# Kernel tuning notes

Hardware: AMD Instinct MI355X
Metric: run time of the kernel (lower is better)

## Reference

```python
import jax, jax.numpy as jnp
import numpy as np

N, C, R, P1, P2 = 8, 3, 8, 512, 512
EPS = 1e-10


def setup_inputs() -> dict:
    key = jax.random.key(0)
    k1, k2, k3, k4 = jax.random.split(key, 4)
    X = jax.random.uniform(k1, (N, C, P1, P2), dtype=jnp.float32)
    S = jax.random.uniform(k2, (C, R), dtype=jnp.float32)
    # mimic the learned-init normalization: unit-norm columns of S
    S = S / jnp.linalg.norm(S, axis=0, keepdims=True)
    gamma = jax.random.uniform(k3, (1,), dtype=jnp.float32) * 1e-5
    lam = jax.random.uniform(k4, (1,), dtype=jnp.float32) * 1e-5
    return {"X": X, "S": S, "gamma": gamma, "lam": lam, "n_iter": 3}


def reference(X, S, gamma, lam, n_iter):
    n, c, p1, p2 = X.shape
    r = S.shape[1]
    p = p1 * p2
    X = X.reshape(n, c, p)
    gamma = jnp.abs(gamma)  # (1,)
    lam = jnp.abs(lam)      # (1,)
    Dt = jnp.zeros((n, r, p), dtype=X.dtype)
    x0 = jnp.mean(X, axis=2, keepdims=True)
    for _ in range(n_iter):
        # ---- D update (proximal gradient) ----
        SDt = jnp.einsum('cr,nrp->ncp', S, Dt)                    # [n,c,p]
        x0 = jnp.mean(X + SDt, axis=2, keepdims=True)             # [n,c,1]
        tau_D = 1.0 / jnp.sum(S * S)                              # 1/||S||_F^2
        Dt = Dt - tau_D * (jnp.einsum('cr,ncp->nrp', S, SDt + X)
                           - jnp.einsum('cr,ncq->nrq', S, x0))
        S_nrm = jnp.linalg.norm(S, axis=0).reshape(1, r, 1)       # col L2 norms of S
        Dt = jax.nn.relu(Dt - lam * gamma * tau_D * S_nrm)        # L1 prox
        Dt_L2 = jnp.linalg.norm(Dt, axis=2, keepdims=True)        # [n,r,1]
        scl = jax.nn.relu(Dt_L2 - lam * tau_D * S_nrm)
        scl = scl / Dt_L2 + EPS                                   # faithful to source
        Dt = Dt * scl                                             # L2 (group) prox
        # ---- S update (proximal gradient) ----
        SDt = jnp.einsum('cr,nrp->ncp', S, Dt)
        x0 = jnp.mean(X + SDt, axis=2, keepdims=True)             # [n,c,1]
        Dt_sum = jnp.sum(Dt, axis=2, keepdims=True)               # [n,r,1]
        tau_S = 1.0 / jnp.mean(jnp.sum(Dt * Dt, axis=(1, 2)))     # 1/mean ||Dt_i||_F^2
        G = (jnp.einsum('ncp,nrp->ncr', SDt + X, Dt)
             - x0 @ jnp.swapaxes(Dt_sum, 1, 2))                   # [n,c,r]
        S_grad = S - tau_S * jnp.mean(G, axis=0)                  # [c,r]
        Dt_nrm = jnp.mean(gamma * jnp.sum(jnp.abs(Dt), axis=2, keepdims=True)
                          + jnp.linalg.norm(Dt, axis=2, keepdims=True), axis=0)  # [r,1]
        S_nrm2 = jnp.linalg.norm(S_grad, axis=0, keepdims=True)   # [1,r]
        scl_S = jax.nn.relu(S_nrm2 - lam * tau_S * Dt_nrm.T)
        scl_S = scl_S / (S_nrm2 + EPS)
        S = S_grad * scl_S
        # ---- unit-norm rescaling of S columns ----
        S_nrm3 = jnp.linalg.norm(S, axis=0, keepdims=True)        # [1,r]
        S = S / (S_nrm3 + EPS)
        Dt = Dt * (S_nrm3.reshape(1, r, 1) + EPS)
    return (x0, S, Dt.reshape(n, r, p1, p2))
```

## Files before the change

### kernel.cpp

```cpp
#include <hip/hip_runtime.h>
#include <math.h>

#define N_ 8
#define C_ 3
#define R_ 8
#define P_ 262144
#define P4_ 65536
#define EPS_ 1e-10f
#define INVP_ (1.0f / (float)P_)
#define NRED 68

#define NBLK_X 64
#define NTHR_  (NBLK_X * 256)
#define NBLK_F 256

#define WS_MXP 0
#define WS_RED 1536
#define WS_POST 3200
#define PSLOT(it) (WS_POST + (it) * 176)
#define WS_DTB 4096
#define WS_NEED_BYTES ((size_t)16384 + (size_t)N_ * R_ * P_ * 2)

struct PostLds {
    float sS[C_][R_];
    float sMx[N_][C_];
    float sTh[R_];
    float sB[N_][R_];
    float sAl[N_][R_];
    float sSumD[N_][R_];
    float sGm[N_][R_][R_ + 1];
    float sXd[N_][C_][R_];
    float sScl[N_][R_];
    float sX0[N_][C_];
    float sTau[1];
};

__device__ __forceinline__ float bf2f(unsigned short s) {
    return __uint_as_float(((unsigned)s) << 16);
}
__device__ __forceinline__ unsigned short f2bf(float f, float* back) {
    unsigned u = __float_as_uint(f);
    unsigned r = (u + 0x7FFFu + ((u >> 16) & 1u)) & 0xFFFF0000u;
    *back = __uint_as_float(r);
    return (unsigned short)(r >> 16);
}

__device__ void prologue(PostLds& L, int it,
                         const float* __restrict__ S_in,
                         const float* __restrict__ gammap,
                         const float* __restrict__ lamp,
                         float* __restrict__ out, float* __restrict__ ws)
{
    const int t = threadIdx.x;
    const int r_l = t & 7, n_l = (t >> 3) & 7;
    const float gamma = fabsf(gammap[0]);
    const float lam   = fabsf(lamp[0]);

    if (t < 24) {
        float s = 0.f;
#pragma unroll
        for (int b = 0; b < 64; ++b) s += ws[WS_MXP + t * 64 + b];
        L.sMx[t / C_][t % C_] = s * INVP_;
    }
    if (t < 24)
        L.sS[t / R_][t % R_] = (it <= 1) ? S_in[t] : ws[PSLOT(it - 1) + t];
    __syncthreads();

    if (it == 0) {
        float ss = 0.f;
#pragma unroll
        for (int c = 0; c < C_; ++c)
#pragma unroll
            for (int rr = 0; rr < R_; ++rr) ss += L.sS[c][rr] * L.sS[c][rr];
        const float tauD0 = 1.f / ss;
        if (t == 0) L.sTau[0] = tauD0;
        if (t < R_) {
            float sn = sqrtf(L.sS[0][t]*L.sS[0][t] + L.sS[1][t]*L.sS[1][t] + L.sS[2][t]*L.sS[2][t]);
            L.sTh[t] = lam * gamma * tauD0 * sn;
        }
        if (t < 64) {
            float b = 0.f;
#pragma unroll
            for (int c = 0; c < C_; ++c) b += L.sS[c][r_l] * L.sMx[n_l][c];
            L.sB[n_l][r_l] = b;
            L.sAl[n_l][r_l] = 0.f;
        }
        __syncthreads();
        return;
    }

    float ssp = 0.f;
#pragma unroll
    for (int c = 0; c < C_; ++c)
#pragma unroll
        for (int rr = 0; rr < R_; ++rr) ssp += L.sS[c][rr] * L.sS[c][rr];
    const float tauDc = 1.f / ssp;

    if (t < 64) {
        const float* red = ws + WS_RED + (size_t)((it - 1) * N_ + n_l) * NRED;
        L.sSumD[n_l][r_l] = red[r_l];
#pragma unroll
        for (int r2 = 0; r2 < R_; ++r2) {
            int hi = r_l > r2 ? r_l : r2, lo = r_l + r2 - hi;
            L.sGm[n_l][r_l][r2] = red[8 + (hi * (hi + 1)) / 2 + lo];
        }
#pragma unroll
        for (int c = 0; c < C_; ++c) L.sXd[n_l][c][r_l] = red[44 + c * R_ + r_l];
    }
    __syncthreads();

    float sc = 0.f, ssq = 0.f, dtn = 0.f, sumD = 0.f;
    if (t < 64) {
        sumD = L.sSumD[n_l][r_l];
        const float snrm = sqrtf(L.sS[0][r_l]*L.sS[0][r_l] + L.sS[1][r_l]*L.sS[1][r_l] + L.sS[2][r_l]*L.sS[2][r_l]);
        const float Gdiag = L.sGm[n_l][r_l][r_l];
        const float L2 = sqrtf(Gdiag);
        sc = fmaxf(L2 - lam * tauDc * snrm, 0.f) / L2 + EPS_;
        L.sScl[n_l][r_l] = sc;
        ssq = sc * sc * Gdiag;
#pragma unroll
        for (int m = 1; m < 64; m <<= 1) ssq += __shfl_xor(ssq, m);
        dtn = gamma * sc * sumD + sc * L2;
#pragma unroll
        for (int m = 8; m < 64; m <<= 1) dtn += __shfl_xor(dtn, m);
    }
    __syncthreads();

    if (t < N_ * C_) {
        int n2 = t / C_, c2 = t % C_;
        float x0 = L.sMx[n2][c2];
#pragma unroll
        for (int rr = 0; rr < R_; ++rr)
            x0 += L.sS[c2][rr] * L.sScl[n2][rr] * L.sSumD[n2][rr] * INVP_;
        L.sX0[n2][c2] = x0;
        if (it == 3) out[t] = x0;
    }
    __syncthreads();

    float Sf[C_] = {0.f, 0.f, 0.f};
    float alpha = 0.f, tauDn = 0.f;
    if (t < 64) {
        float Gc[C_];
#pragma unroll
        for (int c = 0; c < C_; ++c) {
            float tt = 0.f;
#pragma unroll
            for (int r2 = 0; r2 < R_; ++r2)
                tt += L.sS[c][r2] * L.sScl[n_l][r2] * L.sGm[n_l][r2][r_l];
            float G = tt * sc + sc * L.sXd[n_l][c][r_l] - L.sX0[n_l][c] * sc * sumD;
#pragma unroll
            for (int m = 8; m < 64; m <<= 1) G += __shfl_xor(G, m);
            Gc[c] = G;
        }
        const float tauS = (float)N_ / ssq;
        float Sg[C_];
#pragma unroll
        for (int c = 0; c < C_; ++c) Sg[c] = L.sS[c][r_l] - tauS * (Gc[c] / (float)N_);
        const float sn2 = sqrtf(Sg[0]*Sg[0] + Sg[1]*Sg[1] + Sg[2]*Sg[2]);
        const float Dn = dtn / (float)N_;
        const float ssS = fmaxf(sn2 - lam * tauS * Dn, 0.f) / (sn2 + EPS_);
        float s1[C_];
#pragma unroll
        for (int c = 0; c < C_; ++c) s1[c] = Sg[c] * ssS;
        const float sn3 = sqrtf(s1[0]*s1[0] + s1[1]*s1[1] + s1[2]*s1[2]);
#pragma unroll
        for (int c = 0; c < C_; ++c) Sf[c] = s1[c] / (sn3 + EPS_);
        alpha = sc * (sn3 + EPS_);
        float p2 = Sf[0]*Sf[0] + Sf[1]*Sf[1] + Sf[2]*Sf[2];
#pragma unroll
        for (int m = 1; m < 8; m <<= 1) p2 += __shfl_xor(p2, m);
        tauDn = 1.f / p2;
    }
    __syncthreads();
    if (t < 64) {
        L.sAl[n_l][r_l] = alpha;
        if (n_l == 0) {
#pragma unroll
            for (int c = 0; c < C_; ++c) {
                L.sS[c][r_l] = Sf[c];
                if (it == 3) out[24 + c * R_ + r_l] = Sf[c];
            }
            const float snf = sqrtf(Sf[0]*Sf[0] + Sf[1]*Sf[1] + Sf[2]*Sf[2]);
            L.sTh[r_l] = lam * gamma * tauDn * snf;
        }
        if (t == 0) L.sTau[0] = tauDn;
    }
    __syncthreads();
    if (t < 64) {
        float b = 0.f;
#pragma unroll
        for (int c = 0; c < C_; ++c) {
            float x0n = L.sMx[n_l][c];
#pragma unroll
            for (int rr = 0; rr < R_; ++rr)
                x0n += L.sS[c][rr] * L.sAl[n_l][rr] * L.sSumD[n_l][rr] * INVP_;
            b += L.sS[c][r_l] * x0n;
        }
        L.sB[n_l][r_l] = b;
    }
    __syncthreads();
}

__global__ __launch_bounds__(256) void k_post(const float* __restrict__ S_in,
                                              const float* __restrict__ gammap,
                                              const float* __restrict__ lamp,
                                              float* __restrict__ out,
                                              float* __restrict__ ws, int it)
{
    __shared__ PostLds L;
    prologue(L, it, S_in, gammap, lamp, out, ws);
    const int t = threadIdx.x;
    float* slot = ws + PSLOT(it);
    if (t < 24) slot[t] = L.sS[t / R_][t % R_];
    if (t == 24) slot[24] = L.sTau[0];
    if (t < 8) slot[32 + t] = L.sTh[t];
    if (t < 64) {
        slot[40 + t]  = L.sAl[t >> 3][t & 7];
        slot[104 + t] = L.sB[t >> 3][t & 7];
    }
}

__global__ __launch_bounds__(256) void k_meanX(const float* __restrict__ X,
                                               float* __restrict__ ws) {
    const int slice = blockIdx.y;
    const int bx = blockIdx.x;
    const int t = threadIdx.x;
    const int flat = slice * 64 + bx;
    if (flat < 7) {
        int idx = flat * 256 + t;
        if (idx < 3 * N_ * NRED) ws[WS_RED + idx] = 0.f;
    }
    const float4* Xv = (const float4*)(X + (size_t)slice * P_);
    int tid = bx * 256 + t, nthr = 64 * 256;
    float s = 0.f;
    for (int i = tid; i < P4_; i += nthr) {
        float4 v = Xv[i];
        s += v.x + v.y + v.z + v.w;
    }
    for (int off = 32; off; off >>= 1) s += __shfl_down(s, off);
    __shared__ float lds[4];
    int lane = t & 63, wv = t >> 6;
    if (lane == 0) lds[wv] = s;
    __syncthreads();
    if (t == 0) ws[WS_MXP + slice * 64 + bx] = lds[0] + lds[1] + lds[2] + lds[3];
}

template <bool BF16>
__global__ __launch_bounds__(256, 1) void k_pass(
    const float* __restrict__ X,
    float* __restrict__ out, float* __restrict__ ws, int it)
{
    __shared__ float redLds[4][NRED];
    const int t = threadIdx.x, n = blockIdx.y, bx = blockIdx.x;

    const float* ps = ws + PSLOT(it);
    const float tauD = ps[24];
    float Sreg[C_][R_], al[R_], cst[R_];
#pragma unroll
    for (int c = 0; c < C_; ++c)
#pragma unroll
        for (int r = 0; r < R_; ++r) Sreg[c][r] = ps[c * R_ + r];
#pragma unroll
    for (int r = 0; r < R_; ++r) {
        al[r]  = ps[40 + n * R_ + r];
        cst[r] = tauD * ps[104 + n * R_ + r] - ps[32 + r];
    }

    const float4* Xv = (const float4*)(X + (size_t)n * C_ * P_);
    ushort4* Db = (ushort4*)((unsigned short*)(ws + WS_DTB));
    float4*  Df = (float4*)(out + 48);

    float acc[NRED];
#pragma unroll
    for (int k = 0; k < NRED; ++k) acc[k] = 0.f;

    const int tid = bx * 256 + t;
    for (int i = tid; i < P4_; i += NTHR_) {
        float xa[C_][4];
#pragma unroll
        for (int c = 0; c < C_; ++c) {
            float4 v = Xv[(size_t)c * P4_ + i];
            xa[c][0] = v.x; xa[c][1] = v.y; xa[c][2] = v.z; xa[c][3] = v.w;
        }
        float dv[R_][4];
        if (it > 0) {
#pragma unroll
            for (int r = 0; r < R_; ++r) {
                if (BF16) {
                    ushort4 d = Db[(size_t)(n * R_ + r) * P4_ + i];
                    dv[r][0] = bf2f(d.x); dv[r][1] = bf2f(d.y);
                    dv[r][2] = bf2f(d.z); dv[r][3] = bf2f(d.w);
                } else {
                    float4 d = Df[(size_t)(n * R_ + r) * P4_ + i];
                    dv[r][0] = d.x; dv[r][1] = d.y; dv[r][2] = d.z; dv[r][3] = d.w;
                }
            }
        }
#pragma unroll
        for (int q = 0; q < 4; ++q) {
            float ts0 = xa[0][q], ts1 = xa[1][q], ts2 = xa[2][q];
            float v[R_];
#pragma unroll
            for (int r = 0; r < R_; ++r) {
                v[r] = (it > 0) ? al[r] * dv[r][q] : 0.f;
                ts0 += Sreg[0][r] * v[r];
                ts1 += Sreg[1][r] * v[r];
                ts2 += Sreg[2][r] * v[r];
            }
#pragma unroll
            for (int r = 0; r < R_; ++r) {
                float sg = Sreg[0][r]*ts0 + Sreg[1][r]*ts1 + Sreg[2][r]*ts2;
                float u = v[r] - tauD * sg + cst[r];
                dv[r][q] = fmaxf(u, 0.f);
            }
        }
#pragma unroll
        for (int r = 0; r < R_; ++r) {
            if (BF16) {
                ushort4 o;
                o.x = f2bf(dv[r][0], &dv[r][0]);
                o.y = f2bf(dv[r][1], &dv[r][1]);
                o.z = f2bf(dv[r][2], &dv[r][2]);
                o.w = f2bf(dv[r][3], &dv[r][3]);
                Db[(size_t)(n * R_ + r) * P4_ + i] = o;
            } else {
                float4 o;
                o.x = dv[r][0]; o.y = dv[r][1]; o.z = dv[r][2]; o.w = dv[r][3];
                Df[(size_t)(n * R_ + r) * P4_ + i] = o;
            }
        }
#pragma unroll
        for (int r = 0; r < R_; ++r)
            acc[r] += dv[r][0] + dv[r][1] + dv[r][2] + dv[r][3];
#pragma unroll
        for (int r = 0; r < R_; ++r)
#pragma unroll
            for (int r2 = 0; r2 <= r; ++r2)
                acc[8 + (r * (r + 1)) / 2 + r2] +=
                    dv[r][0]*dv[r2][0] + dv[r][1]*dv[r2][1] + dv[r][2]*dv[r2][2] + dv[r][3]*dv[r2][3];
#pragma unroll
        for (int c = 0; c < C_; ++c)
#pragma unroll
            for (int r = 0; r < R_; ++r)
                acc[44 + c * R_ + r] +=
                    xa[c][0]*dv[r][0] + xa[c][1]*dv[r][1] + xa[c][2]*dv[r][2] + xa[c][3]*dv[r][3];
    }

    const int lane = t & 63, wv = t >> 6;
#pragma unroll
    for (int k = 0; k < NRED; ++k) {
        float s = acc[k];
        for (int off = 32; off; off >>= 1) s += __shfl_down(s, off);
        if (lane == 0) redLds[wv][k] = s;
    }
    __syncthreads();
    if (t < NRED)
        atomicAdd(ws + WS_RED + (size_t)(it * N_ + n) * NRED + t,
                  redLds[0][t] + redLds[1][t] + redLds[2][t] + redLds[3][t]);
}

template <bool BF16>
__global__ __launch_bounds__(256) void k_final(
    float* __restrict__ out, const float* __restrict__ ws)
{
    const int t = threadIdx.x, n = blockIdx.y, bx = blockIdx.x;
    const float* ps = ws + PSLOT(3);
    float alv[R_];
#pragma unroll
    for (int r = 0; r < R_; ++r) alv[r] = ps[40 + n * R_ + r];

    const ushort4* Db = (const ushort4*)((const unsigned short*)(ws + WS_DTB));
    float4* Df = (float4*)(out + 48);
    const int i = bx * 256 + t;
#pragma unroll
    for (int r = 0; r < R_; ++r) {
        const float a = alv[r];
        float4 o;
        if (BF16) {
            ushort4 d = Db[(size_t)(n * R_ + r) * P4_ + i];
            o.x = bf2f(d.x) * a; o.y = bf2f(d.y) * a;
            o.z = bf2f(d.z) * a; o.w = bf2f(d.w) * a;
        } else {
            float4 d = Df[(size_t)(n * R_ + r) * P4_ + i];
            o.x = d.x * a; o.y = d.y * a; o.z = d.z * a; o.w = d.w * a;
        }
        Df[(size_t)(n * R_ + r) * P4_ + i] = o;
    }
}

extern "C" void kernel_launch(void* const* d_in, const int* in_sizes, int n_in,
                              void* d_out, int out_size, void* d_ws, size_t ws_size,
                              hipStream_t stream) {
    const float* X     = (const float*)d_in[0];
    const float* S_in  = (const float*)d_in[1];
    const float* gamma = (const float*)d_in[2];
    const float* lam   = (const float*)d_in[3];

    float* out = (float*)d_out;
    float* ws  = (float*)d_ws;

    const bool bf = (ws_size >= WS_NEED_BYTES);

    k_meanX<<<dim3(64, 24), 256, 0, stream>>>(X, ws);
    for (int it = 0; it < 3; ++it) {
        k_post<<<dim3(1, 1), 256, 0, stream>>>(S_in, gamma, lam, out, ws, it);
        if (bf)
            k_pass<true><<<dim3(NBLK_X, N_), 256, 0, stream>>>(X, out, ws, it);
        else
            k_pass<false><<<dim3(NBLK_X, N_), 256, 0, stream>>>(X, out, ws, it);
    }
    k_post<<<dim3(1, 1), 256, 0, stream>>>(S_in, gamma, lam, out, ws, 3);
    if (bf)
        k_final<true><<<dim3(NBLK_F, N_), 256, 0, stream>>>(out, ws);
    else
        k_final<false><<<dim3(NBLK_F, N_), 256, 0, stream>>>(out, ws);
}
```

Measured before the change: 215.2 us.

## Fold single-block post kernel into pass kernel via last-block ticket

Removes the separate single-block k_post launches by having every k_pass block redundantly run the iteration-0 prologue, and by letting the last block to finish each pass (found through an atomic ticket counter) compute the next iteration's parameters. Reduction reads switch to agent-scope atomic loads so the last block sees the other blocks' atomics. This cuts four tiny serial kernel launches and their gaps, at the cost of redundant prologue work in every block at it==0, extra LDS use, and a serialized tail in the last block.

```diff
diff --git a/kernel.cpp b/kernel.cpp
--- a/kernel.cpp
+++ b/kernel.cpp
@@ -16,10 +16,13 @@
 
 #define WS_MXP 0
 #define WS_RED 1536
+#define WS_CNT 3168
 #define WS_POST 3200
 #define PSLOT(it) (WS_POST + (it) * 176)
 #define WS_DTB 4096
 #define WS_NEED_BYTES ((size_t)16384 + (size_t)N_ * R_ * P_ * 2)
+
+#define AGLOAD(p) __hip_atomic_load((p), __ATOMIC_RELAXED, __HIP_MEMORY_SCOPE_AGENT)
 
 struct PostLds {
     float sS[C_][R_];
@@ -98,14 +101,14 @@
 
     if (t < 64) {
         const float* red = ws + WS_RED + (size_t)((it - 1) * N_ + n_l) * NRED;
-        L.sSumD[n_l][r_l] = red[r_l];
+        L.sSumD[n_l][r_l] = AGLOAD(&red[r_l]);
 #pragma unroll
         for (int r2 = 0; r2 < R_; ++r2) {
             int hi = r_l > r2 ? r_l : r2, lo = r_l + r2 - hi;
-            L.sGm[n_l][r_l][r2] = red[8 + (hi * (hi + 1)) / 2 + lo];
-        }
-#pragma unroll
-        for (int c = 0; c < C_; ++c) L.sXd[n_l][c][r_l] = red[44 + c * R_ + r_l];
+            L.sGm[n_l][r_l][r2] = AGLOAD(&red[8 + (hi * (hi + 1)) / 2 + lo]);
+        }
+#pragma unroll
+        for (int c = 0; c < C_; ++c) L.sXd[n_l][c][r_l] = AGLOAD(&red[44 + c * R_ + r_l]);
     }
     __syncthreads();
 
@@ -201,25 +204,6 @@
     __syncthreads();
 }
 
-__global__ __launch_bounds__(256) void k_post(const float* __restrict__ S_in,
-                                              const float* __restrict__ gammap,
-                                              const float* __restrict__ lamp,
-                                              float* __restrict__ out,
-                                              float* __restrict__ ws, int it)
-{
-    __shared__ PostLds L;
-    prologue(L, it, S_in, gammap, lamp, out, ws);
-    const int t = threadIdx.x;
-    float* slot = ws + PSLOT(it);
-    if (t < 24) slot[t] = L.sS[t / R_][t % R_];
-    if (t == 24) slot[24] = L.sTau[0];
-    if (t < 8) slot[32 + t] = L.sTh[t];
-    if (t < 64) {
-        slot[40 + t]  = L.sAl[t >> 3][t & 7];
-        slot[104 + t] = L.sB[t >> 3][t & 7];
-    }
-}
-
 __global__ __launch_bounds__(256) void k_meanX(const float* __restrict__ X,
                                                float* __restrict__ ws) {
     const int slice = blockIdx.y;
@@ -230,6 +214,7 @@
         int idx = flat * 256 + t;
         if (idx < 3 * N_ * NRED) ws[WS_RED + idx] = 0.f;
     }
+    if (flat == 7 && t < 8) ws[WS_CNT + (t & 3)] = 0.f;
     const float4* Xv = (const float4*)(X + (size_t)slice * P_);
     int tid = bx * 256 + t, nthr = 64 * 256;
     float s = 0.f;
@@ -247,23 +232,41 @@
 
 template <bool BF16>
 __global__ __launch_bounds__(256, 1) void k_pass(
-    const float* __restrict__ X,
+    const float* __restrict__ X, const float* __restrict__ S_in,
+    const float* __restrict__ gammap, const float* __restrict__ lamp,
     float* __restrict__ out, float* __restrict__ ws, int it)
 {
+    __shared__ PostLds L;
     __shared__ float redLds[4][NRED];
+    __shared__ int sLast;
     const int t = threadIdx.x, n = blockIdx.y, bx = blockIdx.x;
 
-    const float* ps = ws + PSLOT(it);
-    const float tauD = ps[24];
     float Sreg[C_][R_], al[R_], cst[R_];
-#pragma unroll
-    for (int c = 0; c < C_; ++c)
-#pragma unroll
-        for (int r = 0; r < R_; ++r) Sreg[c][r] = ps[c * R_ + r];
-#pragma unroll
-    for (int r = 0; r < R_; ++r) {
-        al[r]  = ps[40 + n * R_ + r];
-        cst[r] = tauD * ps[104 + n * R_ + r] - ps[32 + r];
+    float tauD;
+    if (it == 0) {
+        prologue(L, 0, S_in, gammap, lamp, out, ws);
+        tauD = L.sTau[0];
+#pragma unroll
+        for (int c = 0; c < C_; ++c)
+#pragma unroll
+            for (int r = 0; r < R_; ++r) Sreg[c][r] = L.sS[c][r];
+#pragma unroll
+        for (int r = 0; r < R_; ++r) {
+            al[r]  = L.sAl[n][r];
+            cst[r] = tauD * L.sB[n][r] - L.sTh[r];
+        }
+    } else {
+        const float* ps = ws + PSLOT(it);
+        tauD = ps[24];
+#pragma unroll
+        for (int c = 0; c < C_; ++c)
+#pragma unroll
+            for (int r = 0; r < R_; ++r) Sreg[c][r] = ps[c * R_ + r];
+#pragma unroll
+        for (int r = 0; r < R_; ++r) {
+            al[r]  = ps[40 + n * R_ + r];
+            cst[r] = tauD * ps[104 + n * R_ + r] - ps[32 + r];
+        }
     }
 
     const float4* Xv = (const float4*)(X + (size_t)n * C_ * P_);
@@ -357,6 +360,27 @@
     if (t < NRED)
         atomicAdd(ws + WS_RED + (size_t)(it * N_ + n) * NRED + t,
                   redLds[0][t] + redLds[1][t] + redLds[2][t] + redLds[3][t]);
+
+    __threadfence();
+    __syncthreads();
+    if (t == 0) {
+        int* cnt = (int*)(ws + WS_CNT) + (it + 1);
+        int ticket = atomicAdd(cnt, 1);
+        sLast = (ticket == NBLK_X * N_ - 1) ? 1 : 0;
+    }
+    __syncthreads();
+    if (sLast) {
+        __threadfence();
+        prologue(L, it + 1, S_in, gammap, lamp, out, ws);
+        float* slot = ws + PSLOT(it + 1);
+        if (t < 24) slot[t] = L.sS[t / R_][t % R_];
+        if (t == 24) slot[24] = L.sTau[0];
+        if (t < 8) slot[32 + t] = L.sTh[t];
+        if (t < 64) {
+            slot[40 + t]  = L.sAl[t >> 3][t & 7];
+            slot[104 + t] = L.sB[t >> 3][t & 7];
+        }
+    }
 }
 
 template <bool BF16>
@@ -403,13 +427,11 @@
 
     k_meanX<<<dim3(64, 24), 256, 0, stream>>>(X, ws);
     for (int it = 0; it < 3; ++it) {
-        k_post<<<dim3(1, 1), 256, 0, stream>>>(S_in, gamma, lam, out, ws, it);
         if (bf)
-            k_pass<true><<<dim3(NBLK_X, N_), 256, 0, stream>>>(X, out, ws, it);
+            k_pass<true><<<dim3(NBLK_X, N_), 256, 0, stream>>>(X, S_in, gamma, lam, out, ws, it);
         else
-            k_pass<false><<<dim3(NBLK_X, N_), 256, 0, stream>>>(X, out, ws, it);
-    }
-    k_post<<<dim3(1, 1), 256, 0, stream>>>(S_in, gamma, lam, out, ws, 3);
+            k_pass<false><<<dim3(NBLK_X, N_), 256, 0, stream>>>(X, S_in, gamma, lam, out, ws, it);
+    }
     if (bf)
         k_final<true><<<dim3(NBLK_F, N_), 256, 0, stream>>>(out, ws);
     else
```

New measurement: 289.9 us. +34.7%, slower.
